# Kernel optimization log

Measured on AMD Instinct MI355X. Metric: run time of the kernel, lower is better.

## Reference

```python
import jax, jax.numpy as jnp
import numpy as np

B, S, DIM = 1, 2048, 4096
NH, NKV, HD = 32, 8, 128  # n_head, n_local_heads (kv heads), head_dim
ROPE_BASE = 10000.0


def setup_inputs() -> dict:
    key = jax.random.key(0)
    k1, k2, k3 = jax.random.split(key, 3)
    x = jax.random.normal(k1, (B, S, DIM), dtype=jnp.float32)
    total_head_dim = (NH + 2 * NKV) * HD  # 6144
    wqkv = jax.random.normal(k2, (total_head_dim, DIM), dtype=jnp.float32) * 0.02
    wo = jax.random.normal(k3, (DIM, DIM), dtype=jnp.float32) * 0.02
    # standard RoPE table: (S, HD//2, 2) = (cos, sin)
    inv_freq = 1.0 / (ROPE_BASE ** (np.arange(0, HD, 2, dtype=np.float32) / HD))
    ang = np.outer(np.arange(S, dtype=np.float32), inv_freq)
    freqs_cis = jnp.asarray(np.stack([np.cos(ang), np.sin(ang)], axis=-1), dtype=jnp.float32)
    return {"x": x, "freqs_cis": freqs_cis, "wqkv": wqkv, "wo": wo}


def _apply_rotary(x, freqs_cis):
    # x: (b, s, h, d); freqs_cis: (s, d//2, 2)
    b, s, h, d = x.shape
    xs = x.reshape(b, s, h, d // 2, 2)
    fc = freqs_cis.reshape(1, s, 1, d // 2, 2)
    re = xs[..., 0] * fc[..., 0] - xs[..., 1] * fc[..., 1]
    im = xs[..., 0] * fc[..., 1] + xs[..., 1] * fc[..., 0]
    return jnp.stack([re, im], axis=-1).reshape(b, s, h, d)


def reference(x, freqs_cis, wqkv, wo):
    b, s, _ = x.shape
    kv_size = NKV * HD
    qkv = x @ wqkv.T  # (b, s, (NH+2*NKV)*HD)
    q, k, v = jnp.split(qkv, [NH * HD, NH * HD + kv_size], axis=-1)
    q = q.reshape(b, s, NH, HD)
    k = k.reshape(b, s, NKV, HD)
    v = v.reshape(b, s, NKV, HD)
    q = _apply_rotary(q, freqs_cis)
    k = _apply_rotary(k, freqs_cis)
    rep = NH // NKV  # GQA expansion factor; repeat_kv == grouped einsum below
    qg = q.reshape(b, s, NKV, rep, HD)
    scale = 1.0 / jnp.sqrt(jnp.asarray(HD, q.dtype))
    # scores: (b, g, r, q_pos, k_pos) -- avoids materializing repeated K/V
    scores = jnp.einsum('bqgrd,bkgd->bgrqk', qg, k) * scale
    causal = jnp.tril(jnp.ones((s, s), dtype=bool))
    scores = jnp.where(causal, scores, jnp.finfo(scores.dtype).min)
    p = jax.nn.softmax(scores, axis=-1)
    o = jnp.einsum('bgrqk,bkgd->bqgrd', p, v).reshape(b, s, NH * HD)
    return o @ wo.T
```

## Files before the change

kernel.cpp:

```cpp
#include <hip/hip_runtime.h>
#include <hip/hip_bf16.h>
#include <math.h>


typedef __attribute__((ext_vector_type(8))) __bf16 bf16x8;
typedef __attribute__((ext_vector_type(4))) __bf16 bf16x4;
typedef __attribute__((ext_vector_type(4))) float f32x4;

#define NEG_BIG (-1e30f)

#define ASYNC_CP16(gsrc, ldst)                                                            \
  __builtin_amdgcn_global_load_lds((const __attribute__((address_space(1))) void*)(gsrc), \
                                   (__attribute__((address_space(3))) void*)(ldst), 16, 0, 0)

__device__ __forceinline__ f32x4 mfma_bf16(bf16x8 a, bf16x8 b, f32x4 c) {
  return __builtin_amdgcn_mfma_f32_16x16x32_bf16(a, b, c, 0, 0, 0);
}

__device__ __forceinline__ float clampf(float v) {
  return fminf(fmaxf(v, -30000.f), 30000.f);
}

__device__ __forceinline__ bf16x8 ldg8(const __hip_bfloat16* p) {
  return *(const bf16x8*)p;
}
__device__ __forceinline__ bf16x8 ldg8(const float* p) {
  f32x4 a = *(const f32x4*)p;
  f32x4 b = *(const f32x4*)(p + 4);
  bf16x8 r;
  r[0] = (__bf16)a[0]; r[1] = (__bf16)a[1]; r[2] = (__bf16)a[2]; r[3] = (__bf16)a[3];
  r[4] = (__bf16)b[0]; r[5] = (__bf16)b[1]; r[6] = (__bf16)b[2]; r[7] = (__bf16)b[3];
  return r;
}

__device__ __forceinline__ void store_c(float* C, size_t idx, float v) {
  C[idx] = clampf(v);
}
__device__ __forceinline__ void store_c(__hip_bfloat16* C, size_t idx, float v) {
  C[idx] = __float2bfloat16(clampf(v));
}

__device__ __forceinline__ void barrier_np() {
  asm volatile("" ::: "memory");
  __builtin_amdgcn_s_barrier();
  asm volatile("" ::: "memory");
}

__global__ __launch_bounds__(256) void cvt_f32_bf16(const float* __restrict__ src,
                                                    __hip_bfloat16* __restrict__ dst) {
  size_t i = ((size_t)blockIdx.x * 256 + threadIdx.x) * 8;
  *(bf16x8*)&dst[i] = ldg8(src + i);
}

__global__ __launch_bounds__(512, 2) void gemm_qkv_rope(
    const __hip_bfloat16* __restrict__ A, const __hip_bfloat16* __restrict__ B,
    __hip_bfloat16* __restrict__ qkv, __hip_bfloat16* __restrict__ vt,
    const float* __restrict__ fc) {
  const int NT = 64;
  __shared__ __align__(16) __hip_bfloat16 lds[4][16384];
  __hip_bfloat16* const As0 = lds[0];
  __hip_bfloat16* const Bs0 = lds[1];
  __hip_bfloat16* const As1 = lds[2];
  __hip_bfloat16* const Bs1 = lds[3];

  const int tid = threadIdx.x;
  const int lane = tid & 63, wid = tid >> 6;
  const int l15 = lane & 15, quad = lane >> 4;
  const int wr = wid >> 2, wc = wid & 3;
  const size_t mBase = (size_t)blockIdx.y * 256, nBase = (size_t)blockIdx.x * 256;

  const int rdOff = l15 * 64 + ((quad * 16) ^ ((l15 & 8) << 2));
  const int wr8 = wr * 8;
  const int wc4 = wc * 4;

  const char* pAsrc[4];
  const char* pBsrc[4];
  int LAel[4], LBel[4];
#pragma unroll
  for (int u = 0; u < 4; ++u) {
    int LA = (tid < 256) ? (4096 * u + tid * 16) : (16384 + 4096 * u + (tid - 256) * 16);
    int LAs = LA ^ (((LA >> 9) & 1) << 5);
    int stA = LAs >> 10, rA16 = (LAs >> 6) & 15, cbA = LAs & 63;
    int rowA = (stA >> 1) * 16 + rA16;
    int colA = (stA & 1) * 32 + (cbA >> 1);
    pAsrc[u] = (const char*)A + ((mBase + rowA) * (size_t)4096 + colA) * 2;
    LAel[u] = LA >> 1;

    int LB = u * 8192 + tid * 16;
    int LBs = LB ^ (((LB >> 9) & 1) << 5);
    int stB = LBs >> 10, rB16 = (LBs >> 6) & 15, cbB = LBs & 63;
    int rowB = (stB >> 1) * 16 + rB16;
    int colB = (stB & 1) * 32 + (cbB >> 1);
    pBsrc[u] = (const char*)B + ((nBase + rowB) * (size_t)4096 + colB) * 2;
    LBel[u] = LB >> 1;
  }

  f32x4 acc[8][4] = {};

#pragma unroll
  for (int u = 0; u < 4; ++u) {
    ASYNC_CP16(pAsrc[u], As0 + LAel[u]);
    ASYNC_CP16(pBsrc[u], Bs0 + LBel[u]);
  }
#pragma unroll
  for (int u = 0; u < 3; ++u) {
    ASYNC_CP16(pAsrc[u] + 128, As1 + LAel[u]);
    ASYNC_CP16(pBsrc[u] + 128, Bs1 + LBel[u]);
  }
  asm volatile("s_waitcnt vmcnt(6)" ::: "memory");
  barrier_np();

#define QKV_TILE(tt, CA, CB, AA, AB)                                                     \
  {                                                                                      \
    bf16x8 bfr[4][2];                                                                    \
    _Pragma("unroll") for (int p = 0; p < 4; ++p) {                                      \
      bf16x8 afr[2][2];                                                                  \
      _Pragma("unroll") for (int ii = 0; ii < 2; ++ii)                                   \
          _Pragma("unroll") for (int kk = 0; kk < 2; ++kk)                               \
              afr[ii][kk] = *(const bf16x8*)((const char*)(CA) +                         \
                                             ((wr8 + 2 * p + ii) * 2048 + kk * 1024 + rdOff)); \
      if (p == 0) {                                                                      \
        _Pragma("unroll") for (int j = 0; j < 4; ++j)                                    \
            _Pragma("unroll") for (int kk = 0; kk < 2; ++kk)                             \
                bfr[j][kk] = *(const bf16x8*)((const char*)(CB) +                        \
                                              ((wc4 + j) * 2048 + kk * 1024 + rdOff));   \
        if ((tt) + 1 < NT) {                                                             \
          ASYNC_CP16(pAsrc[3] + ((tt) + 1) * 128, (AA) + LAel[3]);                       \
          ASYNC_CP16(pBsrc[3] + ((tt) + 1) * 128, (AB) + LBel[3]);                       \
        }                                                                                \
      } else if ((tt) + 2 < NT) {                                                        \
        ASYNC_CP16(pAsrc[p - 1] + ((tt) + 2) * 128, (CA) + LAel[p - 1]);                 \
        ASYNC_CP16(pBsrc[p - 1] + ((tt) + 2) * 128, (CB) + LBel[p - 1]);                 \
      }                                                                                  \
      barrier_np();                                                                      \
      asm volatile("s_waitcnt lgkmcnt(0)" ::: "memory");                                 \
      __builtin_amdgcn_sched_barrier(0);                                                 \
      __builtin_amdgcn_s_setprio(1);                                                     \
      _Pragma("unroll") for (int ii = 0; ii < 2; ++ii)                                   \
          _Pragma("unroll") for (int j = 0; j < 4; ++j)                                  \
              _Pragma("unroll") for (int kk = 0; kk < 2; ++kk)                           \
                  acc[2 * p + ii][j] = mfma_bf16(afr[ii][kk], bfr[j][kk], acc[2 * p + ii][j]); \
      __builtin_amdgcn_s_setprio(0);                                                     \
      if (p == 3) {                                                                      \
        if ((tt) < NT - 2) {                                                             \
          asm volatile("s_waitcnt vmcnt(6)" ::: "memory");                               \
        } else if ((tt) == NT - 2) {                                                     \
          asm volatile("s_waitcnt vmcnt(0)" ::: "memory");                               \
        }                                                                                \
      }                                                                                  \
      barrier_np();                                                                      \
    }                                                                                    \
  }

  for (int t2 = 0; t2 < NT; t2 += 2) {
    QKV_TILE(t2, As0, Bs0, As1, Bs1);
    QKV_TILE(t2 + 1, As1, Bs1, As0, Bs0);
  }
#undef QKV_TILE

#pragma unroll
  for (int i = 0; i < 8; ++i)
#pragma unroll
    for (int j = 0; j < 4; ++j) {
      size_t c = nBase + wc * 64 + j * 16 + l15;
      size_t srow0 = mBase + wr * 128 + i * 16 + quad * 4;
      if (c < 5120) {
        int di2 = (int)(c & 126);
#pragma unroll
        for (int r = 0; r < 4; r++) {
          float v = clampf(acc[i][j][r]);
          float vp = __shfl_xor(v, 1);
          size_t s = srow0 + r;
          float cs = fc[s * 128 + di2];
          float sn = fc[s * 128 + di2 + 1];
          float ov = ((c & 1) == 0) ? (v * cs - vp * sn) : (vp * sn + v * cs);
          qkv[s * 6144 + c] = __float2bfloat16(ov);
        }
      } else {
        bf16x4 pk;
#pragma unroll
        for (int r = 0; r < 4; r++) pk[r] = (__bf16)clampf(acc[i][j][r]);
        *(bf16x4*)&vt[(c - 5120) * 2048 + srow0] = pk;
      }
    }
}

template <typename TC>
__global__ __launch_bounds__(256) void gemm_nt_async(
    const __hip_bfloat16* __restrict__ A, const __hip_bfloat16* __restrict__ B,
    TC* __restrict__ C, int M, int N, int K) {
  __shared__ __align__(16) __hip_bfloat16 As[128 * 32];
  __shared__ __align__(16) __hip_bfloat16 Bs[128 * 32];
  const int tid = threadIdx.x;
  const int lane = tid & 63, wave = tid >> 6;
  const int l15 = lane & 15, quad = lane >> 4;
  const int wm = (wave >> 1) * 64, wn = (wave & 1) * 64;
  const size_t mBase = (size_t)blockIdx.y * 128, nBase = (size_t)blockIdx.x * 128;

  const int ldRow = tid >> 2;
  const int ldCol = (tid & 3) * 8;
  const __hip_bfloat16* Ap = A + (mBase + ldRow) * (size_t)K + ldCol;
  const __hip_bfloat16* Bp = B + (nBase + ldRow) * (size_t)K + ldCol;

  f32x4 acc[4][4] = {};

  for (int k0 = 0; k0 < K; k0 += 32) {
    ASYNC_CP16(Ap, &As[tid * 8]);
    ASYNC_CP16(Ap + (size_t)64 * K, &As[2048 + tid * 8]);
    ASYNC_CP16(Bp, &Bs[tid * 8]);
    ASYNC_CP16(Bp + (size_t)64 * K, &Bs[2048 + tid * 8]);
    Ap += 32; Bp += 32;
    __syncthreads();
    bf16x8 af[4], bfr[4];
#pragma unroll
    for (int i = 0; i < 4; i++)
      af[i] = *(const bf16x8*)&As[(wm + i * 16 + l15) * 32 + quad * 8];
#pragma unroll
    for (int j = 0; j < 4; j++)
      bfr[j] = *(const bf16x8*)&Bs[(wn + j * 16 + l15) * 32 + quad * 8];
#pragma unroll
    for (int i = 0; i < 4; i++)
#pragma unroll
      for (int j = 0; j < 4; j++)
        acc[i][j] = mfma_bf16(af[i], bfr[j], acc[i][j]);
    __syncthreads();
  }

#pragma unroll
  for (int i = 0; i < 4; i++)
#pragma unroll
    for (int j = 0; j < 4; j++)
#pragma unroll
      for (int r = 0; r < 4; r++) {
        size_t row = mBase + wm + i * 16 + quad * 4 + r;
        size_t col = nBase + wn + j * 16 + l15;
        store_c(C, row * (size_t)N + col, acc[i][j][r]);
      }
}

template <typename TA, typename TB, typename TC>
__global__ __launch_bounds__(256) void gemm_nt(
    const TA* __restrict__ A, const TB* __restrict__ B,
    TC* __restrict__ C, int M, int N, int K) {
  __shared__ __align__(16) __hip_bfloat16 As[128 * 32];
  __shared__ __align__(16) __hip_bfloat16 Bs[128 * 32];
  const int tid = threadIdx.x;
  const int lane = tid & 63, wave = tid >> 6;
  const int l15 = lane & 15, quad = lane >> 4;
  const int wm = (wave >> 1) * 64, wn = (wave & 1) * 64;
  const size_t mBase = (size_t)blockIdx.y * 128, nBase = (size_t)blockIdx.x * 128;
  const int ldRow = tid >> 2;
  const int ldCol = (tid & 3) * 8;
  const TA* Ap = A + (mBase + ldRow) * (size_t)K + ldCol;
  const TB* Bp = B + (nBase + ldRow) * (size_t)K + ldCol;
  f32x4 acc[4][4] = {};
  for (int k0 = 0; k0 < K; k0 += 32) {
    bf16x8 a0 = ldg8(Ap);
    bf16x8 a1 = ldg8(Ap + (size_t)64 * K);
    bf16x8 b0 = ldg8(Bp);
    bf16x8 b1 = ldg8(Bp + (size_t)64 * K);
    Ap += 32; Bp += 32;
    *(bf16x8*)&As[tid * 8] = a0;
    *(bf16x8*)&As[2048 + tid * 8] = a1;
    *(bf16x8*)&Bs[tid * 8] = b0;
    *(bf16x8*)&Bs[2048 + tid * 8] = b1;
    __syncthreads();
    bf16x8 af[4], bfr[4];
#pragma unroll
    for (int i = 0; i < 4; i++)
      af[i] = *(const bf16x8*)&As[(wm + i * 16 + l15) * 32 + quad * 8];
#pragma unroll
    for (int j = 0; j < 4; j++)
      bfr[j] = *(const bf16x8*)&Bs[(wn + j * 16 + l15) * 32 + quad * 8];
#pragma unroll
    for (int i = 0; i < 4; i++)
#pragma unroll
      for (int j = 0; j < 4; j++)
        acc[i][j] = mfma_bf16(af[i], bfr[j], acc[i][j]);
    __syncthreads();
  }
#pragma unroll
  for (int i = 0; i < 4; i++)
#pragma unroll
    for (int j = 0; j < 4; j++)
#pragma unroll
      for (int r = 0; r < 4; r++) {
        size_t row = mBase + wm + i * 16 + quad * 4 + r;
        size_t col = nBase + wn + j * 16 + l15;
        store_c(C, row * (size_t)N + col, acc[i][j][r]);
      }
}

__global__ __launch_bounds__(256) void rope_kernel(__hip_bfloat16* __restrict__ qkv,
                                                   const float* __restrict__ fc) {
  int idx = blockIdx.x * 256 + threadIdx.x;
  int d = idx & 63;
  int h = (idx >> 6) % 40;
  int s = idx / (40 * 64);
  size_t off = (size_t)s * 6144 + h * 128 + d * 2;
  float x0 = __bfloat162float(qkv[off]);
  float x1 = __bfloat162float(qkv[off + 1]);
  float c = fc[s * 128 + d * 2];
  float sn = fc[s * 128 + d * 2 + 1];
  qkv[off] = __float2bfloat16(x0 * c - x1 * sn);
  qkv[off + 1] = __float2bfloat16(x0 * sn + x1 * c);
}

__global__ __launch_bounds__(256) void transpose_v(const __hip_bfloat16* __restrict__ qkv,
                                                   __hip_bfloat16* __restrict__ vt) {
  __shared__ __hip_bfloat16 tile[32][33];
  int x = threadIdx.x & 31, y = threadIdx.x >> 5;
  int colBase = blockIdx.x * 32;
  int sBase = blockIdx.y * 32;
#pragma unroll
  for (int i = 0; i < 4; i++)
    tile[y + i * 8][x] = qkv[(size_t)(sBase + y + i * 8) * 6144 + 5120 + colBase + x];
  __syncthreads();
#pragma unroll
  for (int i = 0; i < 4; i++)
    vt[(size_t)(colBase + y + i * 8) * 2048 + sBase + x] = tile[x][y + i * 8];
}

__global__ __launch_bounds__(256) void flash_attn(
    const __hip_bfloat16* __restrict__ qkv, const __hip_bfloat16* __restrict__ vt,
    __hip_bfloat16* __restrict__ o) {
  __shared__ __align__(16) __hip_bfloat16 Ks[64 * 128];
  __shared__ __align__(16) __hip_bfloat16 Vs[128 * 64];
  __shared__ __align__(16) __hip_bfloat16 Ps[4][16 * 72];
  const int tid = threadIdx.x;
  const int lane = tid & 63, wave = tid >> 6;
  const int l15 = lane & 15, quad = lane >> 4;
  const int h = blockIdx.x, g = h >> 2;
  const int qt = 15 - blockIdx.y;
  const int qBase = qt * 128;
  const int qRowW = qBase + wave * 32;

  bf16x8 qf[2][4];
#pragma unroll
  for (int t = 0; t < 2; t++) {
    const __hip_bfloat16* qp =
        qkv + (size_t)(qRowW + t * 16 + l15) * 6144 + h * 128 + quad * 8;
#pragma unroll
    for (int d = 0; d < 4; d++) qf[t][d] = *(const bf16x8*)(qp + d * 32);
  }

  f32x4 acc_o[2][8] = {};
  float m_i[2][4], l_i[2][4];
#pragma unroll
  for (int t = 0; t < 2; t++)
#pragma unroll
    for (int r = 0; r < 4; r++) { m_i[t][r] = NEG_BIG; l_i[t][r] = 0.f; }

  const float scale = 0.08838834764831845f;
  const int nkt = 2 * qt + 2;
  for (int kt = 0; kt < nkt; kt++) {
    const int kBase = kt * 64;
#pragma unroll
    for (int rnd = 0; rnd < 4; rnd++) {
      int ci = rnd * 256 + tid;
      int row = ci >> 4, chl = ci & 15;
      int chg = chl ^ (row & 15);
      ASYNC_CP16(qkv + (size_t)(kBase + row) * 6144 + 4096 + g * 128 + chg * 8, &Ks[ci * 8]);
    }
#pragma unroll
    for (int rnd = 0; rnd < 4; rnd++) {
      int ci = rnd * 256 + tid;
      int n = ci >> 3, chl = ci & 7;
      int chg = chl ^ (n & 7);
      ASYNC_CP16(vt + (size_t)(g * 128 + n) * 2048 + kBase + chg * 8, &Vs[ci * 8]);
    }
    __syncthreads();

    f32x4 sc[2][4] = {};
#pragma unroll
    for (int d = 0; d < 4; d++) {
#pragma unroll
      for (int j = 0; j < 4; j++) {
        bf16x8 kb = *(const bf16x8*)&Ks[(j * 16 + l15) * 128 + ((d * 4 + quad) ^ l15) * 8];
        sc[0][j] = mfma_bf16(qf[0][d], kb, sc[0][j]);
        sc[1][j] = mfma_bf16(qf[1][d], kb, sc[1][j]);
      }
    }

#pragma unroll
    for (int t = 0; t < 2; t++) {
      const int qRowT = qRowW + t * 16;
      float rowmax[4] = {NEG_BIG, NEG_BIG, NEG_BIG, NEG_BIG};
      float sv[4][4];
#pragma unroll
      for (int j = 0; j < 4; j++) {
        int kcol = kBase + j * 16 + l15;
#pragma unroll
        for (int r = 0; r < 4; r++) {
          float s = clampf(sc[t][j][r] * scale);
          if (kcol > qRowT + quad * 4 + r) s = NEG_BIG;
          sv[j][r] = s;
          rowmax[r] = fmaxf(rowmax[r], s);
        }
      }
#pragma unroll
      for (int off = 8; off; off >>= 1)
#pragma unroll
        for (int r = 0; r < 4; r++)
          rowmax[r] = fmaxf(rowmax[r], __shfl_xor(rowmax[r], off, 16));

      float alpha[4], rowsum[4];
#pragma unroll
      for (int r = 0; r < 4; r++) {
        float mnew = fmaxf(m_i[t][r], rowmax[r]);
        alpha[r] = __expf(m_i[t][r] - mnew);
        m_i[t][r] = mnew;
        rowsum[r] = 0.f;
      }
#pragma unroll
      for (int j = 0; j < 4; j++)
#pragma unroll
        for (int r = 0; r < 4; r++) {
          float p = __expf(sv[j][r] - m_i[t][r]);
          rowsum[r] += p;
          Ps[wave][(quad * 4 + r) * 72 + j * 16 + l15] = __float2bfloat16(p);
        }
#pragma unroll
      for (int off = 8; off; off >>= 1)
#pragma unroll
        for (int r = 0; r < 4; r++)
          rowsum[r] += __shfl_xor(rowsum[r], off, 16);
#pragma unroll
      for (int r = 0; r < 4; r++) l_i[t][r] = l_i[t][r] * alpha[r] + rowsum[r];

#pragma unroll
      for (int jt = 0; jt < 8; jt++)
#pragma unroll
        for (int r = 0; r < 4; r++) acc_o[t][jt][r] *= alpha[r];

#pragma unroll
      for (int kk = 0; kk < 2; kk++) {
        bf16x8 pa = *(const bf16x8*)&Ps[wave][l15 * 72 + kk * 32 + quad * 8];
#pragma unroll
        for (int jt = 0; jt < 8; jt++) {
          int n = jt * 16 + l15;
          bf16x8 vb = *(const bf16x8*)&Vs[n * 64 + (((kk * 4 + quad) ^ (n & 7))) * 8];
          acc_o[t][jt] = mfma_bf16(pa, vb, acc_o[t][jt]);
        }
      }
    }
    __syncthreads();
  }

#pragma unroll
  for (int t = 0; t < 2; t++)
#pragma unroll
    for (int r = 0; r < 4; r++) {
      float inv = 1.f / l_i[t][r];
      size_t qr = qRowW + t * 16 + quad * 4 + r;
#pragma unroll
      for (int jt = 0; jt < 8; jt++)
        o[qr * 4096 + h * 128 + jt * 16 + l15] =
            __float2bfloat16(clampf(acc_o[t][jt][r] * inv));
    }
}

extern "C" void kernel_launch(void* const* d_in, const int* in_sizes, int n_in,
                              void* d_out, int out_size, void* d_ws, size_t ws_size,
                              hipStream_t stream) {
  const float* x = (const float*)d_in[0];
  const float* fc = (const float*)d_in[1];
  const float* wqkv = (const float*)d_in[2];
  const float* wo = (const float*)d_in[3];
  float* out = (float*)d_out;

  char* ws = (char*)d_ws;
  __hip_bfloat16* qkv = (__hip_bfloat16*)ws;
  __hip_bfloat16* vt  = (__hip_bfloat16*)(ws + 25165824);
  __hip_bfloat16* ob  = (__hip_bfloat16*)(ws + 29360128);
  __hip_bfloat16* xb  = (__hip_bfloat16*)(ws + 46137344);
  __hip_bfloat16* wb  = (__hip_bfloat16*)(ws + 62914560);

  const bool fast = ws_size >= (size_t)113246208;

  if (fast) {
    cvt_f32_bf16<<<dim3(4096), 256, 0, stream>>>(x, xb);
    cvt_f32_bf16<<<dim3(12288), 256, 0, stream>>>(wqkv, wb);
    gemm_qkv_rope<<<dim3(24, 8), 512, 0, stream>>>(xb, wb, qkv, vt, fc);
  } else {
    gemm_nt<float, float, __hip_bfloat16>
        <<<dim3(48, 16), 256, 0, stream>>>(x, wqkv, qkv, 2048, 6144, 4096);
    rope_kernel<<<dim3(20480), 256, 0, stream>>>(qkv, fc);
    transpose_v<<<dim3(32, 64), 256, 0, stream>>>(qkv, vt);
  }
  flash_attn<<<dim3(32, 16), 256, 0, stream>>>(qkv, vt, ob);
  if (fast) {
    cvt_f32_bf16<<<dim3(8192), 256, 0, stream>>>(wo, wb);
    gemm_nt_async<float>
        <<<dim3(32, 16), 256, 0, stream>>>(ob, wb, out, 2048, 4096, 4096);
  } else {
    gemm_nt<__hip_bfloat16, float, float>
        <<<dim3(32, 16), 256, 0, stream>>>(ob, wo, out, 2048, 4096, 4096);
  }
}
```

Before: 552.7 us.

## Double-buffer K/V tiles, lazy softmax rescale, MFMA row sums in flash attention

Double-buffers the K and V shared-memory tiles so the next tile's async global-to-LDS copy overlaps compute on the current one, which also removes one barrier per iteration. Source pointers are precomputed once, and the query-tile order is reordered to interleave heavy and light causal tiles. The online softmax skips rescaling the accumulators unless the running max grows by more than 8, and row sums are now computed by an MFMA against a vector of ones instead of shuffle reductions. s_setprio is raised around the MFMA sections. These changes double LDS use, which may lower occupancy, and the lazy rescale relies on bounded growth in the fp32 accumulators.

```diff
diff --git a/kernel.cpp b/kernel.cpp
--- a/kernel.cpp
+++ b/kernel.cpp
@@ -324,16 +324,16 @@
 __global__ __launch_bounds__(256) void flash_attn(
     const __hip_bfloat16* __restrict__ qkv, const __hip_bfloat16* __restrict__ vt,
     __hip_bfloat16* __restrict__ o) {
-  __shared__ __align__(16) __hip_bfloat16 Ks[64 * 128];
-  __shared__ __align__(16) __hip_bfloat16 Vs[128 * 64];
+  __shared__ __align__(16) __hip_bfloat16 Ks[2][64 * 128];
+  __shared__ __align__(16) __hip_bfloat16 Vs[2][128 * 64];
   __shared__ __align__(16) __hip_bfloat16 Ps[4][16 * 72];
   const int tid = threadIdx.x;
   const int lane = tid & 63, wave = tid >> 6;
   const int l15 = lane & 15, quad = lane >> 4;
   const int h = blockIdx.x, g = h >> 2;
-  const int qt = 15 - blockIdx.y;
-  const int qBase = qt * 128;
-  const int qRowW = qBase + wave * 32;
+  const int y = blockIdx.y;
+  const int qt = (y < 8) ? (15 - y) : (y - 8);
+  const int qRowW = qt * 128 + wave * 32;
 
   bf16x8 qf[2][4];
 #pragma unroll
@@ -344,43 +344,68 @@
     for (int d = 0; d < 4; d++) qf[t][d] = *(const bf16x8*)(qp + d * 32);
   }
 
+  const __hip_bfloat16* kSrc[4];
+  const __hip_bfloat16* vSrc[4];
+  int sOff[4];
+#pragma unroll
+  for (int rnd = 0; rnd < 4; rnd++) {
+    int ci = rnd * 256 + tid;
+    int row = ci >> 4, chl = ci & 15;
+    int chg = chl ^ (row & 15);
+    kSrc[rnd] = qkv + (size_t)row * 6144 + 4096 + g * 128 + chg * 8;
+    int n = ci >> 3, ch2 = ci & 7;
+    int cg2 = ch2 ^ (n & 7);
+    vSrc[rnd] = vt + (size_t)(g * 128 + n) * 2048 + cg2 * 8;
+    sOff[rnd] = ci * 8;
+  }
+
   f32x4 acc_o[2][8] = {};
-  float m_i[2][4], l_i[2][4];
+  f32x4 rs[2] = {};
+  float m_i[2][4];
 #pragma unroll
   for (int t = 0; t < 2; t++)
 #pragma unroll
-    for (int r = 0; r < 4; r++) { m_i[t][r] = NEG_BIG; l_i[t][r] = 0.f; }
+    for (int r = 0; r < 4; r++) m_i[t][r] = NEG_BIG;
+
+  bf16x8 ones;
+#pragma unroll
+  for (int i = 0; i < 8; i++) ones[i] = (__bf16)1.0f;
 
   const float scale = 0.08838834764831845f;
   const int nkt = 2 * qt + 2;
+  int cur = 0;
+
+#pragma unroll
+  for (int rnd = 0; rnd < 4; rnd++) {
+    ASYNC_CP16(kSrc[rnd], &Ks[0][sOff[rnd]]);
+    ASYNC_CP16(vSrc[rnd], &Vs[0][sOff[rnd]]);
+  }
+
   for (int kt = 0; kt < nkt; kt++) {
     const int kBase = kt * 64;
-#pragma unroll
-    for (int rnd = 0; rnd < 4; rnd++) {
-      int ci = rnd * 256 + tid;
-      int row = ci >> 4, chl = ci & 15;
-      int chg = chl ^ (row & 15);
-      ASYNC_CP16(qkv + (size_t)(kBase + row) * 6144 + 4096 + g * 128 + chg * 8, &Ks[ci * 8]);
+    __syncthreads();
+
+    if (kt + 1 < nkt) {
+      const size_t ko = (size_t)(kBase + 64);
+#pragma unroll
+      for (int rnd = 0; rnd < 4; rnd++) {
+        ASYNC_CP16(kSrc[rnd] + ko * 6144, &Ks[cur ^ 1][sOff[rnd]]);
+        ASYNC_CP16(vSrc[rnd] + ko, &Vs[cur ^ 1][sOff[rnd]]);
+      }
     }
-#pragma unroll
-    for (int rnd = 0; rnd < 4; rnd++) {
-      int ci = rnd * 256 + tid;
-      int n = ci >> 3, chl = ci & 7;
-      int chg = chl ^ (n & 7);
-      ASYNC_CP16(vt + (size_t)(g * 128 + n) * 2048 + kBase + chg * 8, &Vs[ci * 8]);
-    }
-    __syncthreads();
 
     f32x4 sc[2][4] = {};
+    __builtin_amdgcn_s_setprio(1);
 #pragma unroll
     for (int d = 0; d < 4; d++) {
 #pragma unroll
       for (int j = 0; j < 4; j++) {
-        bf16x8 kb = *(const bf16x8*)&Ks[(j * 16 + l15) * 128 + ((d * 4 + quad) ^ l15) * 8];
+        bf16x8 kb = *(const bf16x8*)&Ks[cur][(j * 16 + l15) * 128 + ((d * 4 + quad) ^ l15) * 8];
         sc[0][j] = mfma_bf16(qf[0][d], kb, sc[0][j]);
         sc[1][j] = mfma_bf16(qf[1][d], kb, sc[1][j]);
       }
     }
+    __builtin_amdgcn_s_setprio(0);
 
 #pragma unroll
     for (int t = 0; t < 2; t++) {
@@ -404,54 +429,54 @@
         for (int r = 0; r < 4; r++)
           rowmax[r] = fmaxf(rowmax[r], __shfl_xor(rowmax[r], off, 16));
 
-      float alpha[4], rowsum[4];
-#pragma unroll
-      for (int r = 0; r < 4; r++) {
-        float mnew = fmaxf(m_i[t][r], rowmax[r]);
-        alpha[r] = __expf(m_i[t][r] - mnew);
-        m_i[t][r] = mnew;
-        rowsum[r] = 0.f;
-      }
+      bool ok = (rowmax[0] <= m_i[t][0] + 8.f) & (rowmax[1] <= m_i[t][1] + 8.f) &
+                (rowmax[2] <= m_i[t][2] + 8.f) & (rowmax[3] <= m_i[t][3] + 8.f);
+      if (!__all(ok)) {
+        float alpha[4];
+#pragma unroll
+        for (int r = 0; r < 4; r++) {
+          float mnew = fmaxf(m_i[t][r], rowmax[r]);
+          alpha[r] = __expf(m_i[t][r] - mnew);
+          m_i[t][r] = mnew;
+        }
+#pragma unroll
+        for (int jt = 0; jt < 8; jt++)
+#pragma unroll
+          for (int r = 0; r < 4; r++) acc_o[t][jt][r] *= alpha[r];
+#pragma unroll
+        for (int r = 0; r < 4; r++) rs[t][r] *= alpha[r];
+      }
+
 #pragma unroll
       for (int j = 0; j < 4; j++)
 #pragma unroll
         for (int r = 0; r < 4; r++) {
           float p = __expf(sv[j][r] - m_i[t][r]);
-          rowsum[r] += p;
           Ps[wave][(quad * 4 + r) * 72 + j * 16 + l15] = __float2bfloat16(p);
         }
-#pragma unroll
-      for (int off = 8; off; off >>= 1)
-#pragma unroll
-        for (int r = 0; r < 4; r++)
-          rowsum[r] += __shfl_xor(rowsum[r], off, 16);
-#pragma unroll
-      for (int r = 0; r < 4; r++) l_i[t][r] = l_i[t][r] * alpha[r] + rowsum[r];
-
-#pragma unroll
-      for (int jt = 0; jt < 8; jt++)
-#pragma unroll
-        for (int r = 0; r < 4; r++) acc_o[t][jt][r] *= alpha[r];
-
+
+      __builtin_amdgcn_s_setprio(1);
 #pragma unroll
       for (int kk = 0; kk < 2; kk++) {
         bf16x8 pa = *(const bf16x8*)&Ps[wave][l15 * 72 + kk * 32 + quad * 8];
+        rs[t] = mfma_bf16(pa, ones, rs[t]);
 #pragma unroll
         for (int jt = 0; jt < 8; jt++) {
           int n = jt * 16 + l15;
-          bf16x8 vb = *(const bf16x8*)&Vs[n * 64 + (((kk * 4 + quad) ^ (n & 7))) * 8];
+          bf16x8 vb = *(const bf16x8*)&Vs[cur][n * 64 + (((kk * 4 + quad) ^ (n & 7))) * 8];
           acc_o[t][jt] = mfma_bf16(pa, vb, acc_o[t][jt]);
         }
       }
+      __builtin_amdgcn_s_setprio(0);
     }
-    __syncthreads();
+    cur ^= 1;
   }
 
 #pragma unroll
   for (int t = 0; t < 2; t++)
 #pragma unroll
     for (int r = 0; r < 4; r++) {
-      float inv = 1.f / l_i[t][r];
+      float inv = 1.f / rs[t][r];
       size_t qr = qRowW + t * 16 + quad * 4 + r;
 #pragma unroll
       for (int jt = 0; jt < 8; jt++)
```

New measurement: 576.8 us. 4.4% more time.
